# Performance work log

Measured on AMD Instinct MI355X. Metric: run time of the kernel, lower is better.

Reference implementation:

```python
import jax, jax.numpy as jnp
import numpy as np

N_HEADS = 16


def setup_inputs() -> dict:
    key = jax.random.key(0)
    ks = jax.random.split(key, 9)
    B, S, D = 2, 2048, 1024
    sc = 0.02
    return {
        'x': jax.random.normal(ks[0], (B, S, D), jnp.float32),
        'Wq': jax.random.normal(ks[1], (D, D), jnp.float32) * sc,
        'bq': jax.random.normal(ks[2], (D,), jnp.float32) * sc,
        'Wk': jax.random.normal(ks[3], (D, D), jnp.float32) * sc,
        'bk': jax.random.normal(ks[4], (D,), jnp.float32) * sc,
        'Wv': jax.random.normal(ks[5], (D, D), jnp.float32) * sc,
        'bv': jax.random.normal(ks[6], (D,), jnp.float32) * sc,
        'Wo': jax.random.normal(ks[7], (D, D), jnp.float32) * sc,
        'bo': jax.random.normal(ks[8], (D,), jnp.float32) * sc,
    }


def reference(x, Wq, bq, Wk, bk, Wv, bv, Wo, bo):
    # Chunked causal prefill. The chunk-wise mask (q_pos >= kv_pos over the
    # growing KV cache) is mathematically identical to full causal attention,
    # so we compute it as one vectorized masked softmax attention.
    B, S, D = x.shape
    H = N_HEADS
    hd = D // H

    def proj(W, b):
        # torch Linear: y = x @ W.T + b ; then split heads -> [B,H,S,hd]
        y = jnp.einsum('bsd,ed->bse', x, W) + b
        return y.reshape(B, S, H, hd).transpose(0, 2, 1, 3)

    q = proj(Wq, bq)
    k = proj(Wk, bk)
    v = proj(Wv, bv)

    scores = jnp.einsum('bhqd,bhkd->bhqk', q, k) / jnp.sqrt(jnp.asarray(hd, x.dtype))
    causal = jnp.tril(jnp.ones((S, S), dtype=bool))  # [S,S]
    scores = jnp.where(causal[None, None], scores, jnp.asarray(-jnp.inf, scores.dtype))
    attn = jax.nn.softmax(scores, axis=-1)
    ctx = jnp.einsum('bhqk,bhkd->bhqd', attn, v)  # [B,H,S,hd]
    ctx = ctx.transpose(0, 2, 1, 3).reshape(B, S, D)
    out = jnp.einsum('bsd,ed->bse', ctx, Wo) + bo
    return out
```

## Files before the change

### kernel.cpp

```cpp
#include <hip/hip_runtime.h>
#include <cstdint>
#include <math.h>

typedef _Float16 f16;
typedef _Float16 f16x2 __attribute__((ext_vector_type(2)));
typedef _Float16 f16x4 __attribute__((ext_vector_type(4)));
typedef _Float16 f16x8 __attribute__((ext_vector_type(8)));
typedef __fp16   h16x2 __attribute__((ext_vector_type(2)));
typedef float    f32x4 __attribute__((ext_vector_type(4)));

__device__ __forceinline__ f32x4 mfma16(f16x8 a, f16x8 b, f32x4 c) {
  return __builtin_amdgcn_mfma_f32_16x16x32_f16(a, b, c, 0, 0, 0);
}
__device__ __forceinline__ void gl2lds16(const f16* g, f16* l) {
  __builtin_amdgcn_global_load_lds((__attribute__((address_space(1))) void*)(g),
                                   (__attribute__((address_space(3))) void*)(l),
                                   16, 0, 0);
}
__device__ __forceinline__ float fexp2(float x) { return __builtin_amdgcn_exp2f(x); }
__device__ __forceinline__ f16x2 pkrtz(float a, float b) {
  h16x2 r = __builtin_amdgcn_cvt_pkrtz(a, b);
  return __builtin_bit_cast(f16x2, r);
}
__device__ __forceinline__ float dot2acc(f16x2 a, f16x2 b, float c) {
#if __has_builtin(__builtin_amdgcn_fdot2)
  return __builtin_amdgcn_fdot2(__builtin_bit_cast(h16x2, a),
                                __builtin_bit_cast(h16x2, b), c, false);
#else
  return c + (float)a[0] * (float)b[0] + (float)a[1] * (float)b[1];
#endif
}

__global__ __launch_bounds__(256) void cvt_kernel(
    const float* __restrict__ x,  const float* __restrict__ wq, const float* __restrict__ wk,
    const float* __restrict__ wv, const float* __restrict__ wo,
    f16* __restrict__ xh, f16* __restrict__ wqkvh, f16* __restrict__ woh)
{
  const int seg = blockIdx.y;
  const float* src; f16* dst; int n;
  if      (seg == 0) { src = x;  dst = xh;              n = 4194304; }
  else if (seg == 1) { src = wq; dst = wqkvh;           n = 1048576; }
  else if (seg == 2) { src = wk; dst = wqkvh + 1048576; n = 1048576; }
  else if (seg == 3) { src = wv; dst = wqkvh + 2097152; n = 1048576; }
  else               { src = wo; dst = woh;             n = 1048576; }
  const int idx = (int)(blockIdx.x * 256 + threadIdx.x) * 8;
  if (idx >= n) return;
  f32x4 a = *(const f32x4*)(src + idx);
  f32x4 b = *(const f32x4*)(src + idx + 4);
  f16x8 h;
  h[0] = (f16)a[0]; h[1] = (f16)a[1]; h[2] = (f16)a[2]; h[3] = (f16)a[3];
  h[4] = (f16)b[0]; h[5] = (f16)b[1]; h[6] = (f16)b[2]; h[7] = (f16)b[3];
  *(f16x8*)(dst + idx) = h;
}

__global__ __launch_bounds__(256) void gemm_qkv(
    const f16* __restrict__ A, const f16* __restrict__ B,
    const float* __restrict__ bias0, const float* __restrict__ bias1, const float* __restrict__ bias2,
    f16* __restrict__ Qp, f16* __restrict__ Kp, f16* __restrict__ Vp)
{
  constexpr int K = 1024;
  __shared__ __align__(16) f16 As[128 * 32];
  __shared__ __align__(16) f16 Bs[128 * 32];
  const int tid  = threadIdx.x;
  const int wave = tid >> 6, lane = tid & 63;
  const int quad = lane >> 4, col = lane & 15;
  const int tile_m = blockIdx.y * 128, tile_n = blockIdx.x * 128;
  const int mb = (wave >> 1) * 64, nb = (wave & 1) * 64;
  const int srow = lane >> 2, scol = (lane & 3) * 8;
  const f16* gA = A + (size_t)(tile_m + wave * 32 + srow) * K + scol;
  const f16* gB = B + (size_t)(tile_n + wave * 32 + srow) * K + scol;
  f16* lA = As + wave * 1024;
  f16* lB = Bs + wave * 1024;

  f32x4 acc[4][4] = {};
  for (int k0 = 0; k0 < K; k0 += 32) {
    gl2lds16(gA + k0,          lA);
    gl2lds16(gA + 16 * K + k0, lA + 512);
    gl2lds16(gB + k0,          lB);
    gl2lds16(gB + 16 * K + k0, lB + 512);
    __syncthreads();
    f16x8 af[4], bf[4];
    #pragma unroll
    for (int i = 0; i < 4; ++i)
      af[i] = *(const f16x8*)&As[(mb + i * 16 + col) * 32 + quad * 8];
    #pragma unroll
    for (int j = 0; j < 4; ++j)
      bf[j] = *(const f16x8*)&Bs[(nb + j * 16 + col) * 32 + quad * 8];
    #pragma unroll
    for (int i = 0; i < 4; ++i)
      #pragma unroll
      for (int j = 0; j < 4; ++j)
        acc[i][j] = mfma16(af[i], bf[j], acc[i][j]);
    __syncthreads();
  }

  #pragma unroll
  for (int j = 0; j < 4; ++j) {
    const int gn = tile_n + nb + j * 16 + col;
    const int which = gn >> 10;
    const int d = gn & 1023;
    const float* bp = (which == 0) ? bias0 : (which == 1) ? bias1 : bias2;
    f16* dst        = (which == 0) ? Qp    : (which == 1) ? Kp    : Vp;
    const float bvv = bp[d];
    const float qs  = (which == 0) ? 0.18033688f : 1.0f;
    const int h = d >> 6, hi = d & 63;
    #pragma unroll
    for (int i = 0; i < 4; ++i) {
      #pragma unroll
      for (int r = 0; r < 4; ++r) {
        const int gm = tile_m + mb + i * 16 + quad * 4 + r;
        const int bb = gm >> 11, s = gm & 2047;
        dst[(((size_t)bb * 16 + h) * 2048 + s) * 64 + hi] = (f16)((acc[i][j][r] + bvv) * qs);
      }
    }
  }
}

__global__ __launch_bounds__(256) void vtrans_kernel(
    const f16* __restrict__ Vh, f16* __restrict__ Vt)
{
  __shared__ __align__(16) f16 t[64][72];
  const int bh = blockIdx.y;
  const int s0 = blockIdx.x * 64;
  const int tid = threadIdx.x;
  const int sr = tid >> 2, dc = (tid & 3) * 16;
  const size_t ib = ((size_t)bh * 2048 + s0 + sr) * 64 + dc;
  f16x8 v0 = *(const f16x8*)&Vh[ib];
  f16x8 v1 = *(const f16x8*)&Vh[ib + 8];
  *(f16x8*)&t[sr][dc]     = v0;
  *(f16x8*)&t[sr][dc + 8] = v1;
  __syncthreads();
  const int d = tid >> 2, sc = (tid & 3) * 16;
  f16x8 o0, o1;
  #pragma unroll
  for (int j = 0; j < 8; ++j) { o0[j] = t[sc + j][d]; o1[j] = t[sc + 8 + j][d]; }
  const size_t ob = ((size_t)bh * 64 + d) * 2048 + s0 + sc;
  *(f16x8*)&Vt[ob]     = o0;
  *(f16x8*)&Vt[ob + 8] = o1;
}

__global__ __launch_bounds__(256) void attn_kernel(
    const f16* __restrict__ Q, const f16* __restrict__ K, const f16* __restrict__ Vt,
    f16* __restrict__ ctx)
{
  __shared__ __align__(16) f16 Ks[64 * 72];
  __shared__ __align__(16) f16 Vts[64 * 72];
  __shared__ __align__(16) f16 Ps[4][16 * 72];
  __shared__ __align__(16) float abuf[4][16];
  __shared__ __align__(16) float lbuf[4][16];

  const int bh  = blockIdx.y;
  const int tid = threadIdx.x;
  const int wave = tid >> 6, lane = tid & 63;
  const int quad = lane >> 4, col = lane & 15;
  const int b = bh >> 4, h = bh & 15;
  const size_t base = (size_t)bh * 2048 * 64;
  const size_t vtb  = (size_t)bh * 64 * 2048;

  int srow[2], sc8[2];
  #pragma unroll
  for (int i = 0; i < 2; ++i) {
    const int flat = tid + i * 256;
    srow[i] = flat >> 3;
    sc8[i]  = (flat & 7) * 8;
  }

  auto run_tile = [&](int qt) {
    const int q0 = qt * 64;
    const int qa = q0 + wave * 16;
    const f16x8 bqa0 = *(const f16x8*)&Q[base + (size_t)(qa + col) * 64 + quad * 8];
    const f16x8 bqa1 = *(const f16x8*)&Q[base + (size_t)(qa + col) * 64 + 32 + quad * 8];

    f32x4 cta[4] = {};
    float ma = -INFINITY, la = 0.f;

    f16x8 kr[2], vr[2];
    auto gload = [&](int t) {
      #pragma unroll
      for (int i = 0; i < 2; ++i) {
        kr[i] = *(const f16x8*)&K[base + (size_t)(t * 64 + srow[i]) * 64 + sc8[i]];
        vr[i] = *(const f16x8*)&Vt[vtb + (size_t)srow[i] * 2048 + t * 64 + sc8[i]];
      }
    };
    gload(0);

    const int nIter = qt + 1;
    for (int t = 0; t < nIter; ++t) {
      __syncthreads();
      #pragma unroll
      for (int i = 0; i < 2; ++i) {
        *(f16x8*)&Ks[srow[i] * 72 + sc8[i]]  = kr[i];
        *(f16x8*)&Vts[srow[i] * 72 + sc8[i]] = vr[i];
      }
      __syncthreads();
      if (t + 1 < nIter) gload(t + 1);

      f32x4 sa[4];
      #pragma unroll
      for (int jt = 0; jt < 4; ++jt) {
        const int kro = (jt * 16 + col) * 72;
        const f16x8 ak0 = *(const f16x8*)&Ks[kro + quad * 8];
        const f16x8 ak1 = *(const f16x8*)&Ks[kro + 32 + quad * 8];
        f32x4 za = {};
        za = mfma16(ak0, bqa0, za);
        sa[jt] = mfma16(ak1, bqa1, za);
      }

      if (t == qt) {
        #pragma unroll
        for (int jt = 0; jt < 4; ++jt) {
          const int kg = t * 64 + jt * 16 + quad * 4;
          #pragma unroll
          for (int r = 0; r < 4; ++r) {
            if (kg + r > qa + col) sa[jt][r] = -1e30f;
          }
        }
      }

      const f16x2 one2 = {(_Float16)1.f, (_Float16)1.f};
      {
        float tm = fmaxf(fmaxf(sa[0][0], sa[0][1]), fmaxf(sa[0][2], sa[0][3]));
        #pragma unroll
        for (int jt = 1; jt < 4; ++jt)
          tm = fmaxf(tm, fmaxf(fmaxf(sa[jt][0], sa[jt][1]), fmaxf(sa[jt][2], sa[jt][3])));
        tm = fmaxf(tm, __shfl_xor(tm, 16));
        tm = fmaxf(tm, __shfl_xor(tm, 32));
        const float mnew = fmaxf(ma, tm);
        const float alpha = fexp2(ma - mnew);
        ma = mnew;
        float rs = 0.f;
        #pragma unroll
        for (int jt = 0; jt < 4; ++jt) {
          const f16x2 a01 = pkrtz(fexp2(sa[jt][0] - mnew), fexp2(sa[jt][1] - mnew));
          const f16x2 a23 = pkrtz(fexp2(sa[jt][2] - mnew), fexp2(sa[jt][3] - mnew));
          rs = dot2acc(a01, one2, rs);
          rs = dot2acc(a23, one2, rs);
          f16x4 pw; pw[0] = a01[0]; pw[1] = a01[1]; pw[2] = a23[0]; pw[3] = a23[1];
          *(f16x4*)&Ps[wave][col * 72 + jt * 16 + quad * 4] = pw;
        }
        rs += __shfl_xor(rs, 16);
        rs += __shfl_xor(rs, 32);
        la = la * alpha + rs;
        if (quad == 0) abuf[wave][col] = alpha;
      }

      __asm__ volatile("s_waitcnt lgkmcnt(0)" ::: "memory");
      const f32x4 ava = *(const f32x4*)&abuf[wave][quad * 4];
      #pragma unroll
      for (int jd = 0; jd < 4; ++jd) cta[jd] *= ava;

      const f16x8 apa0 = *(const f16x8*)&Ps[wave][col * 72 + quad * 8];
      const f16x8 apa1 = *(const f16x8*)&Ps[wave][col * 72 + 32 + quad * 8];
      #pragma unroll
      for (int jd = 0; jd < 4; ++jd) {
        const int vro = (jd * 16 + col) * 72;
        const f16x8 bv0 = *(const f16x8*)&Vts[vro + quad * 8];
        const f16x8 bv1 = *(const f16x8*)&Vts[vro + 32 + quad * 8];
        cta[jd] = mfma16(apa1, bv1, mfma16(apa0, bv0, cta[jd]));
      }
    }

    if (quad == 0) lbuf[wave][col] = la;
    __asm__ volatile("s_waitcnt lgkmcnt(0)" ::: "memory");
    const f32x4 lva = *(const f32x4*)&lbuf[wave][quad * 4];
    #pragma unroll
    for (int jd = 0; jd < 4; ++jd) {
      #pragma unroll
      for (int r = 0; r < 4; ++r) {
        const int qga = qa + quad * 4 + r;
        const int d = h * 64 + jd * 16 + col;
        ctx[((size_t)b * 2048 + qga) * 1024 + d] = (f16)(cta[jd][r] / lva[r]);
      }
    }
  };

  run_tile(blockIdx.x);
  run_tile(31 - blockIdx.x);
}

__global__ __launch_bounds__(256) void gemm_o(
    const f16* __restrict__ A, const f16* __restrict__ B, const float* __restrict__ bias,
    float* __restrict__ Out)
{
  constexpr int K = 1024;
  __shared__ __align__(16) f16 As[128 * 32];
  __shared__ __align__(16) f16 Bs[64 * 32];
  const int tid  = threadIdx.x;
  const int wave = tid >> 6, lane = tid & 63;
  const int quad = lane >> 4, col = lane & 15;
  const int tile_m = blockIdx.y * 128, tile_n = blockIdx.x * 64;
  const int mb = wave * 32;
  const int srow = lane >> 2, scol = (lane & 3) * 8;
  const f16* gA = A + (size_t)(tile_m + wave * 32 + srow) * K + scol;
  const f16* gB = B + (size_t)(tile_n + wave * 16 + srow) * K + scol;
  f16* lA = As + wave * 1024;
  f16* lB = Bs + wave * 512;

  f32x4 acc[2][4] = {};
  for (int k0 = 0; k0 < K; k0 += 32) {
    gl2lds16(gA + k0,          lA);
    gl2lds16(gA + 16 * K + k0, lA + 512);
    gl2lds16(gB + k0,          lB);
    __syncthreads();
    f16x8 af[2], bf[4];
    #pragma unroll
    for (int i = 0; i < 2; ++i)
      af[i] = *(const f16x8*)&As[(mb + i * 16 + col) * 32 + quad * 8];
    #pragma unroll
    for (int j = 0; j < 4; ++j)
      bf[j] = *(const f16x8*)&Bs[(j * 16 + col) * 32 + quad * 8];
    #pragma unroll
    for (int i = 0; i < 2; ++i)
      #pragma unroll
      for (int j = 0; j < 4; ++j)
        acc[i][j] = mfma16(af[i], bf[j], acc[i][j]);
    __syncthreads();
  }

  #pragma unroll
  for (int j = 0; j < 4; ++j) {
    const int gn = tile_n + j * 16 + col;
    const float bvv = bias[gn];
    #pragma unroll
    for (int i = 0; i < 2; ++i) {
      #pragma unroll
      for (int r = 0; r < 4; ++r) {
        const int gm = tile_m + mb + i * 16 + quad * 4 + r;
        Out[(size_t)gm * 1024 + gn] = acc[i][j][r] + bvv;
      }
    }
  }
}

extern "C" void kernel_launch(void* const* d_in, const int* in_sizes, int n_in,
                              void* d_out, int out_size, void* d_ws, size_t ws_size,
                              hipStream_t stream)
{
  const float* x  = (const float*)d_in[0];
  const float* Wq = (const float*)d_in[1];
  const float* bq = (const float*)d_in[2];
  const float* Wk = (const float*)d_in[3];
  const float* bk = (const float*)d_in[4];
  const float* Wv = (const float*)d_in[5];
  const float* bv = (const float*)d_in[6];
  const float* Wo = (const float*)d_in[7];
  const float* bo = (const float*)d_in[8];
  float* out = (float*)d_out;

  f16* ws = (f16*)d_ws;
  const size_t M1 = 1048576;
  f16* xh    = ws;
  f16* wqkvh = ws + 4  * M1;
  f16* woh   = ws + 7  * M1;
  f16* Qh    = ws + 8  * M1;
  f16* Kh    = ws + 12 * M1;
  f16* Vh    = ws + 16 * M1;
  f16* Vth   = ws + 20 * M1;
  f16* ctxh  = ws + 24 * M1;

  cvt_kernel<<<dim3(2048, 5), 256, 0, stream>>>(x, Wq, Wk, Wv, Wo, xh, wqkvh, woh);
  gemm_qkv<<<dim3(24, 32), 256, 0, stream>>>(xh, wqkvh, bq, bk, bv, Qh, Kh, Vh);
  vtrans_kernel<<<dim3(32, 32), 256, 0, stream>>>(Vh, Vth);
  attn_kernel<<<dim3(16, 32), 256, 0, stream>>>(Qh, Kh, Vth, ctxh);
  gemm_o<<<dim3(16, 32), 256, 0, stream>>>(ctxh, woh, bo, out);
}
```

Before: 197.4 us.

## Load K/V fragments directly from global into registers, drop LDS staging and barriers

The attention kernel no longer stages K and Vt tiles through shared memory with block-wide barriers. Each wave now loads its own MFMA operand fragments straight from global memory: K is prefetched one iteration ahead and V is loaded at the start of each iteration. The alpha and l row-scale broadcasts move from LDS round-trips to lane shuffles. This removes the __syncthreads pairs and the LDS writes, but each of the 4 waves now reads the full K/V tile from global/L2 (4x redundant traffic), with more register pressure and V load latency less hidden.

```diff
diff --git a/kernel.cpp b/kernel.cpp
--- a/kernel.cpp
+++ b/kernel.cpp
@@ -143,11 +143,7 @@
     const f16* __restrict__ Q, const f16* __restrict__ K, const f16* __restrict__ Vt,
     f16* __restrict__ ctx)
 {
-  __shared__ __align__(16) f16 Ks[64 * 72];
-  __shared__ __align__(16) f16 Vts[64 * 72];
   __shared__ __align__(16) f16 Ps[4][16 * 72];
-  __shared__ __align__(16) float abuf[4][16];
-  __shared__ __align__(16) float lbuf[4][16];
 
   const int bh  = blockIdx.y;
   const int tid = threadIdx.x;
@@ -157,13 +153,8 @@
   const size_t base = (size_t)bh * 2048 * 64;
   const size_t vtb  = (size_t)bh * 64 * 2048;
 
-  int srow[2], sc8[2];
-  #pragma unroll
-  for (int i = 0; i < 2; ++i) {
-    const int flat = tid + i * 256;
-    srow[i] = flat >> 3;
-    sc8[i]  = (flat & 7) * 8;
-  }
+  const f16* Kb = K + base + (size_t)col * 64 + quad * 8;
+  const f16* Vb = Vt + vtb + (size_t)col * 2048 + quad * 8;
 
   auto run_tile = [&](int qt) {
     const int q0 = qt * 64;
@@ -174,37 +165,36 @@
     f32x4 cta[4] = {};
     float ma = -INFINITY, la = 0.f;
 
-    f16x8 kr[2], vr[2];
-    auto gload = [&](int t) {
-      #pragma unroll
-      for (int i = 0; i < 2; ++i) {
-        kr[i] = *(const f16x8*)&K[base + (size_t)(t * 64 + srow[i]) * 64 + sc8[i]];
-        vr[i] = *(const f16x8*)&Vt[vtb + (size_t)srow[i] * 2048 + t * 64 + sc8[i]];
+    f16x8 kf[8];
+    auto loadK = [&](int t) {
+      #pragma unroll
+      for (int jt = 0; jt < 4; ++jt) {
+        const f16* p = Kb + ((size_t)t * 64 + jt * 16) * 64;
+        kf[2 * jt]     = *(const f16x8*)(p);
+        kf[2 * jt + 1] = *(const f16x8*)(p + 32);
       }
     };
-    gload(0);
+    loadK(0);
 
     const int nIter = qt + 1;
     for (int t = 0; t < nIter; ++t) {
-      __syncthreads();
-      #pragma unroll
-      for (int i = 0; i < 2; ++i) {
-        *(f16x8*)&Ks[srow[i] * 72 + sc8[i]]  = kr[i];
-        *(f16x8*)&Vts[srow[i] * 72 + sc8[i]] = vr[i];
-      }
-      __syncthreads();
-      if (t + 1 < nIter) gload(t + 1);
+      f16x8 vf[8];
+      #pragma unroll
+      for (int jd = 0; jd < 4; ++jd) {
+        const f16* p = Vb + (size_t)(jd * 16) * 2048 + t * 64;
+        vf[2 * jd]     = *(const f16x8*)(p);
+        vf[2 * jd + 1] = *(const f16x8*)(p + 32);
+      }
 
       f32x4 sa[4];
       #pragma unroll
       for (int jt = 0; jt < 4; ++jt) {
-        const int kro = (jt * 16 + col) * 72;
-        const f16x8 ak0 = *(const f16x8*)&Ks[kro + quad * 8];
-        const f16x8 ak1 = *(const f16x8*)&Ks[kro + 32 + quad * 8];
         f32x4 za = {};
-        za = mfma16(ak0, bqa0, za);
-        sa[jt] = mfma16(ak1, bqa1, za);
-      }
+        za = mfma16(kf[2 * jt], bqa0, za);
+        sa[jt] = mfma16(kf[2 * jt + 1], bqa1, za);
+      }
+
+      if (t + 1 < nIter) loadK(t + 1);
 
       if (t == qt) {
         #pragma unroll
@@ -218,6 +208,7 @@
       }
 
       const f16x2 one2 = {(_Float16)1.f, (_Float16)1.f};
+      float alpha;
       {
         float tm = fmaxf(fmaxf(sa[0][0], sa[0][1]), fmaxf(sa[0][2], sa[0][3]));
         #pragma unroll
@@ -226,7 +217,7 @@
         tm = fmaxf(tm, __shfl_xor(tm, 16));
         tm = fmaxf(tm, __shfl_xor(tm, 32));
         const float mnew = fmaxf(ma, tm);
-        const float alpha = fexp2(ma - mnew);
+        alpha = fexp2(ma - mnew);
         ma = mnew;
         float rs = 0.f;
         #pragma unroll
@@ -241,28 +232,26 @@
         rs += __shfl_xor(rs, 16);
         rs += __shfl_xor(rs, 32);
         la = la * alpha + rs;
-        if (quad == 0) abuf[wave][col] = alpha;
-      }
+      }
+
+      f32x4 ava;
+      #pragma unroll
+      for (int r = 0; r < 4; ++r) ava[r] = __shfl(alpha, quad * 4 + r);
+      #pragma unroll
+      for (int jd = 0; jd < 4; ++jd) cta[jd] *= ava;
 
       __asm__ volatile("s_waitcnt lgkmcnt(0)" ::: "memory");
-      const f32x4 ava = *(const f32x4*)&abuf[wave][quad * 4];
-      #pragma unroll
-      for (int jd = 0; jd < 4; ++jd) cta[jd] *= ava;
 
       const f16x8 apa0 = *(const f16x8*)&Ps[wave][col * 72 + quad * 8];
       const f16x8 apa1 = *(const f16x8*)&Ps[wave][col * 72 + 32 + quad * 8];
       #pragma unroll
-      for (int jd = 0; jd < 4; ++jd) {
-        const int vro = (jd * 16 + col) * 72;
-        const f16x8 bv0 = *(const f16x8*)&Vts[vro + quad * 8];
-        const f16x8 bv1 = *(const f16x8*)&Vts[vro + 32 + quad * 8];
-        cta[jd] = mfma16(apa1, bv1, mfma16(apa0, bv0, cta[jd]));
-      }
+      for (int jd = 0; jd < 4; ++jd)
+        cta[jd] = mfma16(apa1, vf[2 * jd + 1], mfma16(apa0, vf[2 * jd], cta[jd]));
     }
 
-    if (quad == 0) lbuf[wave][col] = la;
-    __asm__ volatile("s_waitcnt lgkmcnt(0)" ::: "memory");
-    const f32x4 lva = *(const f32x4*)&lbuf[wave][quad * 4];
+    f32x4 lva;
+    #pragma unroll
+    for (int r = 0; r < 4; ++r) lva[r] = __shfl(la, quad * 4 + r);
     #pragma unroll
     for (int jd = 0; jd < 4; ++jd) {
       #pragma unroll
```

Measured after the change: 265.2 us. +34.3%, slower.
